# Kernel tuning notes

Measured on AMD Instinct MI355X. Metric: run time of the kernel, lower is better.

## Reference

```python
import jax, jax.numpy as jnp
import numpy as np

EPS = 1e-5
B, C, H, W = 64, 256, 64, 64


def _masked_mean(p9, r0, r1, c0, c1):
    # p9: [B,3,3,9,H,W]; r0,r1: [B,3] int row bounds (per i); c0,c1: [B,3] int col bounds (per j)
    Hh, Ww = p9.shape[-2], p9.shape[-1]
    rows = jnp.arange(Hh, dtype=jnp.int32)
    cols = jnp.arange(Ww, dtype=jnp.int32)
    mr = (rows[None, None, :] >= r0[..., None]) & (rows[None, None, :] < r1[..., None])  # [B,3,H]
    mc = (cols[None, None, :] >= c0[..., None]) & (cols[None, None, :] < c1[..., None])  # [B,3,W]
    mask = (mr[:, :, None, :, None] & mc[:, None, :, None, :]).astype(p9.dtype)  # [B,3,3,H,W]
    cnt = mask.sum((-2, -1))  # [B,3,3]
    s = jnp.einsum('bijkhw,bijhw->bijk', p9, mask)
    return jnp.where(cnt[..., None] > 0, s / jnp.maximum(cnt, 1.0)[..., None], 0.0)  # [B,3,3,9]


def _subj_obj_bounds(bbox, Hh, Ww):
    # bbox: [B,4] = [y0,y1,x0,x1] normalized
    y0, y1, x0, x1 = bbox[:, 0], bbox[:, 1], bbox[:, 2], bbox[:, 3]
    ch = (y1 - y0) / 3.0
    cw = (x1 - x0) / 3.0
    idx = jnp.arange(3, dtype=bbox.dtype)
    r0 = jnp.floor(Hh * (y0[:, None] + idx * ch[:, None])).astype(jnp.int32)
    r1 = jnp.floor(Hh * (y0[:, None] + (idx + 1.0) * ch[:, None])).astype(jnp.int32)
    dr = r1 <= r0
    r1n = jnp.where(dr & (r1 < Hh - 1), r1 + 1, r1)
    r0n = jnp.where(dr & (r1 >= Hh - 1), r0 - 1, r0)
    c0 = jnp.floor(Ww * (x0[:, None] + idx * cw[:, None])).astype(jnp.int32)
    c1 = jnp.floor(Ww * (x0[:, None] + (idx + 1.0) * cw[:, None])).astype(jnp.int32)
    dc = c1 <= c0
    c1n = jnp.where(dc & (c1 < Ww), c1 + 1, c1)
    c0n = jnp.where(dc & (c1 >= Ww), c0 - 1, c0)
    return r0n, r1n, c0n, c1n


def _joint_bounds(bbox, bbox_s, bbox_o, Hh, Ww):
    # intersection of bbox with the 3x3 cells of union(bbox_s, bbox_o)
    uy0 = jnp.minimum(bbox_s[:, 0], bbox_o[:, 0])
    uy1 = jnp.maximum(bbox_s[:, 1], bbox_o[:, 1])
    ux0 = jnp.minimum(bbox_s[:, 2], bbox_o[:, 2])
    ux1 = jnp.maximum(bbox_s[:, 3], bbox_o[:, 3])
    ch = (uy1 - uy0) / 3.0
    cw = (ux1 - ux0) / 3.0
    idx = jnp.arange(3, dtype=bbox.dtype)
    ylo = uy0[:, None] + idx * ch[:, None]
    yhi = uy0[:, None] + (idx + 1.0) * ch[:, None]
    xlo = ux0[:, None] + idx * cw[:, None]
    xhi = ux0[:, None] + (idx + 1.0) * cw[:, None]
    r0 = jnp.floor(Hh * jnp.maximum(bbox[:, 0][:, None], ylo)).astype(jnp.int32)
    r1 = jnp.floor(Hh * jnp.minimum(bbox[:, 1][:, None], yhi)).astype(jnp.int32)
    c0 = jnp.floor(Ww * jnp.maximum(bbox[:, 2][:, None], xlo)).astype(jnp.int32)
    c1 = jnp.floor(Ww * jnp.minimum(bbox[:, 3][:, None], xhi)).astype(jnp.int32)
    return r0, r1, c0, c1


def setup_inputs() -> dict:
    key = jax.random.key(0)
    ks = jax.random.split(key, 16)
    feat = jax.random.normal(ks[0], (B, C, H, W), dtype=jnp.float32)

    def make_bbox(k):
        k1, k2, k3, k4 = jax.random.split(k, 4)
        y0 = jax.random.uniform(k1, (B,), minval=0.0, maxval=0.4)
        y1 = jnp.minimum(y0 + jax.random.uniform(k2, (B,), minval=0.3, maxval=0.55), 0.99)
        x0 = jax.random.uniform(k3, (B,), minval=0.0, maxval=0.4)
        x1 = jnp.minimum(x0 + jax.random.uniform(k4, (B,), minval=0.3, maxval=0.55), 0.99)
        return jnp.stack([y0, y1, x0, x1], axis=1).astype(jnp.float32)

    bbox_s = make_bbox(ks[1])
    bbox_o = make_bbox(ks[2])
    predicate = jax.random.uniform(ks[3], (B, 9), dtype=jnp.float32)
    conv_w = jax.random.normal(ks[4], (324, 256), dtype=jnp.float32) * 0.02
    conv_b = jax.random.normal(ks[5], (324,), dtype=jnp.float32) * 0.02
    bn2_g = jax.random.uniform(ks[6], (324,), minval=0.5, maxval=1.5)
    bn2_b = jax.random.normal(ks[7], (324,)) * 0.02
    bn2_m = jax.random.normal(ks[8], (324,)) * 0.02
    bn2_v = jax.random.uniform(ks[9], (324,), minval=0.5, maxval=1.5)
    fc1_w = jax.random.normal(ks[10], (40, 81), dtype=jnp.float32) * 0.1
    fc1_b = jnp.zeros((40,), jnp.float32)
    bn1_g = jax.random.uniform(ks[11], (40,), minval=0.5, maxval=1.5)
    bn1_b = jax.random.normal(ks[12], (40,)) * 0.02
    bn1_m = jax.random.normal(ks[13], (40,)) * 0.02
    bn1_v = jax.random.uniform(ks[14], (40,), minval=0.5, maxval=1.5)
    fc2_w = jax.random.normal(ks[15], (9, 40), dtype=jnp.float32) * 0.1
    fc2_b = jnp.zeros((9,), jnp.float32)
    return dict(feat=feat, bbox_s=bbox_s, bbox_o=bbox_o, predicate=predicate,
                conv_w=conv_w, conv_b=conv_b, bn2_g=bn2_g, bn2_b=bn2_b, bn2_m=bn2_m, bn2_v=bn2_v,
                fc1_w=fc1_w, fc1_b=fc1_b, bn1_g=bn1_g, bn1_b=bn1_b, bn1_m=bn1_m, bn1_v=bn1_v,
                fc2_w=fc2_w, fc2_b=fc2_b)


def reference(feat, bbox_s, bbox_o, predicate, conv_w, conv_b, bn2_g, bn2_b, bn2_m, bn2_v,
              fc1_w, fc1_b, bn1_g, bn1_b, bn1_m, bn1_v, fc2_w, fc2_b):
    # 1x1 conv 256 -> 324, then BatchNorm2d (inference mode)
    prs = jnp.einsum('bchw,oc->bohw', feat, conv_w) + conv_b[None, :, None, None]
    prs = (prs - bn2_m[None, :, None, None]) * (bn2_g / jnp.sqrt(bn2_v + EPS))[None, :, None, None] + bn2_b[None, :, None, None]
    Bb, _, Hh, Ww = prs.shape
    # channel layout: start = i*27 + j*9 + k  ->  reshape to [B,3,3,9,H,W]
    def bank(lo):
        return prs[:, lo:lo + 81].reshape(Bb, 3, 3, 9, Hh, Ww)
    prs_s, prs_o, prs_js, prs_jo = bank(0), bank(81), bank(162), bank(243)

    feature_s = _masked_mean(prs_s, *_subj_obj_bounds(bbox_s, Hh, Ww))
    feature_o = _masked_mean(prs_o, *_subj_obj_bounds(bbox_o, Hh, Ww))
    feature_j = (_masked_mean(prs_js, *_joint_bounds(bbox_s, bbox_s, bbox_o, Hh, Ww)) +
                 _masked_mean(prs_jo, *_joint_bounds(bbox_o, bbox_s, bbox_o, Hh, Ww)))

    f = feature_s + feature_o + feature_j            # [B,3,3,9]
    f = jnp.transpose(f, (0, 3, 1, 2)).reshape(Bb, 81)  # torch layout [B,9,3,3] flattened

    h = f @ fc1_w.T + fc1_b
    h = (h - bn1_m) * (bn1_g / jnp.sqrt(bn1_v + EPS)) + bn1_b
    logits = h @ fc2_w.T + fc2_b
    return jnp.sum(logits * predicate, axis=1)
```

## Files before the change

kernel.cpp:

```cpp
#include <hip/hip_runtime.h>
#include <hip/hip_bf16.h>
#include <cstdint>

#define BB 64
#define CC 256
#define EPSF 1e-5f
#define PLANES 8
#define ZROW 24
#define SSTR 65
#define NPLANES (BB * CC)

__device__ __forceinline__ void region_bounds(int bank, int i, int j,
                                              float sy0, float sy1, float sx0, float sx1,
                                              float oy0, float oy1, float ox0, float ox1,
                                              int& r0, int& r1, int& c0, int& c1) {
    float fi = (float)i, fj = (float)j;
    if (bank < 2) {
        float y0 = bank ? oy0 : sy0, y1 = bank ? oy1 : sy1;
        float x0 = bank ? ox0 : sx0, x1 = bank ? ox1 : sx1;
        float ch = __fdiv_rn(__fsub_rn(y1, y0), 3.0f);
        float cw = __fdiv_rn(__fsub_rn(x1, x0), 3.0f);
        int R0 = (int)floorf(__fmul_rn(64.0f, __fadd_rn(y0, __fmul_rn(fi, ch))));
        int R1 = (int)floorf(__fmul_rn(64.0f, __fadd_rn(y0, __fmul_rn(__fadd_rn(fi, 1.0f), ch))));
        bool dr = (R1 <= R0);
        r1 = (dr && (R1 < 63)) ? R1 + 1 : R1;
        r0 = (dr && (R1 >= 63)) ? R0 - 1 : R0;
        int C0 = (int)floorf(__fmul_rn(64.0f, __fadd_rn(x0, __fmul_rn(fj, cw))));
        int C1 = (int)floorf(__fmul_rn(64.0f, __fadd_rn(x0, __fmul_rn(__fadd_rn(fj, 1.0f), cw))));
        bool dc = (C1 <= C0);
        c1 = (dc && (C1 < 64)) ? C1 + 1 : C1;
        c0 = (dc && (C1 >= 64)) ? C0 - 1 : C0;
    } else {
        float by0 = (bank == 2) ? sy0 : oy0, by1 = (bank == 2) ? sy1 : oy1;
        float bx0 = (bank == 2) ? sx0 : ox0, bx1 = (bank == 2) ? sx1 : ox1;
        float uy0 = fminf(sy0, oy0), uy1 = fmaxf(sy1, oy1);
        float ux0 = fminf(sx0, ox0), ux1 = fmaxf(sx1, ox1);
        float ch = __fdiv_rn(__fsub_rn(uy1, uy0), 3.0f);
        float cw = __fdiv_rn(__fsub_rn(ux1, ux0), 3.0f);
        float ylo = __fadd_rn(uy0, __fmul_rn(fi, ch));
        float yhi = __fadd_rn(uy0, __fmul_rn(__fadd_rn(fi, 1.0f), ch));
        float xlo = __fadd_rn(ux0, __fmul_rn(fj, cw));
        float xhi = __fadd_rn(ux0, __fmul_rn(__fadd_rn(fj, 1.0f), cw));
        r0 = (int)floorf(__fmul_rn(64.0f, fmaxf(by0, ylo)));
        r1 = (int)floorf(__fmul_rn(64.0f, fminf(by1, yhi)));
        c0 = (int)floorf(__fmul_rn(64.0f, fmaxf(bx0, xlo)));
        c1 = (int)floorf(__fmul_rn(64.0f, fminf(bx1, xhi)));
    }
}

__global__ __launch_bounds__(64, 4) void k_region_sums(const float* __restrict__ feat,
                                                       const float* __restrict__ bbox_s,
                                                       const float* __restrict__ bbox_o,
                                                       float* __restrict__ M) {
    int l = threadIdx.x;
    int pid0 = blockIdx.x * PLANES;
    int b = pid0 >> 8;

    float sy0 = bbox_s[b * 4 + 0], sy1 = bbox_s[b * 4 + 1];
    float sx0 = bbox_s[b * 4 + 2], sx1 = bbox_s[b * 4 + 3];
    float oy0 = bbox_o[b * 4 + 0], oy1 = bbox_o[b * 4 + 1];
    float ox0 = bbox_o[b * 4 + 2], ox1 = bbox_o[b * 4 + 3];

    int myb = l / 9, rest = l % 9, myi = rest / 3, myj = rest % 3;

    unsigned long long needm = 0ull, snapm = 0ull;
    int my_r0c = 0, my_r1c = 0, mycl = 0, mych = 0;
    bool colact = false;
    int cmin = 64;
    #pragma unroll
    for (int bk = 0; bk < 4; ++bk) {
        #pragma unroll
        for (int idx = 0; idx < 3; ++idx) {
            int r0, r1, c0, c1;
            region_bounds(bk, idx, idx, sy0, sy1, sx0, sx1, oy0, oy1, ox0, ox1,
                          r0, r1, c0, c1);
            int r0c = max(r0, 0), r1c = min(r1, 64);
            if (r1c > r0c) {
                unsigned long long hi = (r1c >= 64) ? ~0ull : ((1ull << r1c) - 1ull);
                unsigned long long lo = (1ull << r0c) - 1ull;
                needm |= hi ^ lo;
                snapm |= 1ull << (r1c - 1);
                if (r0c >= 1) snapm |= 1ull << (r0c - 1);
            }
            int clc = max(c0, 0), chc = min(c1, 64);
            if (chc > clc) {
                colact = colact || (l >= clc && l < chc);
                cmin = min(cmin, clc);
            }
            if (bk == myb && idx == myi) { my_r0c = r0c; my_r1c = r1c; }
            if (bk == myb && idx == myj) { mycl = max(c0, 0); mych = min(c1, 64); }
        }
    }
    {
        unsigned int a = __builtin_amdgcn_readfirstlane((unsigned int)needm);
        unsigned int bm = __builtin_amdgcn_readfirstlane((unsigned int)(needm >> 32));
        needm = (((unsigned long long)bm) << 32) | a;
        unsigned int c = __builtin_amdgcn_readfirstlane((unsigned int)snapm);
        unsigned int d = __builtin_amdgcn_readfirstlane((unsigned int)(snapm >> 32));
        snapm = (((unsigned long long)d) << 32) | c;
    }
    if (cmin >= 64) cmin = 0;
    int col_tgt = colact ? l : cmin;

    int cl = 0, chx = 0, idx0 = ZROW, idx1 = ZROW;
    if (l < 36) {
        cl = mycl; chx = mych;
        if (my_r1c <= my_r0c) {
            chx = cl;
        } else {
            idx1 = (int)__popcll(snapm & ((1ull << (my_r1c - 1)) - 1ull));
            idx0 = (my_r0c > 0) ? (int)__popcll(snapm & ((1ull << (my_r0c - 1)) - 1ull))
                                : ZROW;
        }
    }

    __shared__ float S[(ZROW + 1) * SSTR];
    S[ZROW * SSTR + l] = 0.0f;
    asm volatile("s_waitcnt lgkmcnt(0)" ::: "memory");

    const float* pfbase = feat + (size_t)pid0 * 4096 + col_tgt;
    float xA[32], xB[32];
    float run = 0.0f;
    int slot = 0;

#define ISSUE_H(X, Q)                                                       \
    do {                                                                    \
        const float* pp = pfbase + (size_t)((Q) >> 1) * 4096;               \
        const int h0 = ((Q) & 1) * 32;                                      \
        _Pragma("unroll")                                                   \
        for (int h = 0; h < 32; ++h) {                                      \
            if ((needm >> (h0 + h)) & 1ull) X[h] = pp[(h0 + h) * 64];       \
        }                                                                   \
    } while (0)

#define CONSUME_H(X, Q)                                                     \
    do {                                                                    \
        const int h0 = ((Q) & 1) * 32;                                      \
        if (h0 == 0) { run = 0.0f; slot = 0; }                              \
        _Pragma("unroll")                                                   \
        for (int h = 0; h < 32; ++h) {                                      \
            if ((needm >> (h0 + h)) & 1ull) run += X[h];                    \
            if ((snapm >> (h0 + h)) & 1ull) { S[slot * SSTR + l] = run; ++slot; } \
        }                                                                   \
    } while (0)

#define EVALP(P)                                                            \
    do {                                                                    \
        asm volatile("s_waitcnt lgkmcnt(0)" ::: "memory");                  \
        if (l < 36) {                                                       \
            float s = 0.0f;                                                 \
            for (int w = cl; w < chx; ++w)                                  \
                s += S[idx1 * SSTR + w] - S[idx0 * SSTR + w];               \
            M[(size_t)l * NPLANES + pid0 + (P)] = s;                        \
        }                                                                   \
        asm volatile("" ::: "memory");                                      \
    } while (0)

    ISSUE_H(xA, 0); ISSUE_H(xB, 1);
    CONSUME_H(xA, 0);  ISSUE_H(xA, 2);
    CONSUME_H(xB, 1);  ISSUE_H(xB, 3);   EVALP(0);
    CONSUME_H(xA, 2);  ISSUE_H(xA, 4);
    CONSUME_H(xB, 3);  ISSUE_H(xB, 5);   EVALP(1);
    CONSUME_H(xA, 4);  ISSUE_H(xA, 6);
    CONSUME_H(xB, 5);  ISSUE_H(xB, 7);   EVALP(2);
    CONSUME_H(xA, 6);  ISSUE_H(xA, 8);
    CONSUME_H(xB, 7);  ISSUE_H(xB, 9);   EVALP(3);
    CONSUME_H(xA, 8);  ISSUE_H(xA, 10);
    CONSUME_H(xB, 9);  ISSUE_H(xB, 11);  EVALP(4);
    CONSUME_H(xA, 10); ISSUE_H(xA, 12);
    CONSUME_H(xB, 11); ISSUE_H(xB, 13);  EVALP(5);
    CONSUME_H(xA, 12); ISSUE_H(xA, 14);
    CONSUME_H(xB, 13); ISSUE_H(xB, 15);  EVALP(6);
    CONSUME_H(xA, 14);
    CONSUME_H(xB, 15);                   EVALP(7);

#undef ISSUE_H
#undef CONSUME_H
#undef EVALP
}

__global__ __launch_bounds__(128) void k_head_dot(const float* __restrict__ M,
                                                  const float* __restrict__ bbox_s,
                                                  const float* __restrict__ bbox_o,
                                                  const float* __restrict__ conv_w,
                                                  const float* __restrict__ conv_b,
                                                  const float* __restrict__ g2,
                                                  const float* __restrict__ b2,
                                                  const float* __restrict__ m2,
                                                  const float* __restrict__ v2,
                                                  float* __restrict__ val) {
    int blk = blockIdx.x;
    int b = blk >> 2, bank = blk & 3;
    int t = threadIdx.x;

    __shared__ float MlT9[9 * 264];
    for (int i = t; i < 9 * 256; i += 128) {
        int ij = i >> 8, c = i & 255;
        MlT9[ij * 264 + c] = M[(size_t)(bank * 9 + ij) * NPLANES + (b << 8) + c];
    }
    __syncthreads();

    if (t < 81) {
        int ij = t / 9, k = t - ij * 9;
        int ii = ij / 3, jj = ij % 3;
        int o = bank * 81 + ii * 27 + jj * 9 + k;

        float sy0 = bbox_s[b * 4 + 0], sy1 = bbox_s[b * 4 + 1];
        float sx0 = bbox_s[b * 4 + 2], sx1 = bbox_s[b * 4 + 3];
        float oy0 = bbox_o[b * 4 + 0], oy1 = bbox_o[b * 4 + 1];
        float ox0 = bbox_o[b * 4 + 2], ox1 = bbox_o[b * 4 + 3];
        int r0, r1, c0, c1;
        region_bounds(bank, ii, jj, sy0, sy1, sx0, sx1, oy0, oy1, ox0, ox1,
                      r0, r1, c0, c1);
        int nrows = max(0, min(r1, 64) - max(r0, 0));
        int ncols = max(0, min(c1, 64) - max(c0, 0));
        float cnt = (float)(nrows * ncols);

        float v = 0.0f;
        if (cnt > 0.0f) {
            const float4* wv = (const float4*)(conv_w + o * 256);
            const float4* mv = (const float4*)(&MlT9[ij * 264]);
            float4 a4 = make_float4(0.f, 0.f, 0.f, 0.f);
            #pragma unroll 8
            for (int c4 = 0; c4 < 64; ++c4) {
                float4 wq = wv[c4], mq = mv[c4];
                a4.x += wq.x * mq.x; a4.y += wq.y * mq.y;
                a4.z += wq.z * mq.z; a4.w += wq.w * mq.w;
            }
            float dot = (a4.x + a4.y) + (a4.z + a4.w);
            float mean = dot / cnt;
            float sc = g2[o] / sqrtf(v2[o] + EPSF);
            v = (mean + conv_b[o] - m2[o]) * sc + b2[o];
        }
        val[b * 324 + bank * 81 + t] = v;
    }
}

__global__ __launch_bounds__(128) void k_head_mlp(const float* __restrict__ val,
                                                  const float* __restrict__ fc1_w,
                                                  const float* __restrict__ fc1_b,
                                                  const float* __restrict__ g1,
                                                  const float* __restrict__ b1,
                                                  const float* __restrict__ m1,
                                                  const float* __restrict__ v1,
                                                  const float* __restrict__ fc2_w,
                                                  const float* __restrict__ fc2_b,
                                                  const float* __restrict__ pred,
                                                  float* __restrict__ out) {
    int b = blockIdx.x;
    int t = threadIdx.x;

    __shared__ float fv[81];
    __shared__ float hv[40];
    __shared__ float lg[9];

    if (t < 81) {
        int k = t / 9, ij = t - k * 9;
        const float* vb = val + b * 324;
        fv[t] = vb[0 * 81 + ij * 9 + k] + vb[1 * 81 + ij * 9 + k] +
                vb[2 * 81 + ij * 9 + k] + vb[3 * 81 + ij * 9 + k];
    }
    __syncthreads();

    if (t < 40) {
        float h = fc1_b[t];
        for (int u = 0; u < 81; ++u) h += fv[u] * fc1_w[t * 81 + u];
        h = (h - m1[t]) * (g1[t] / sqrtf(v1[t] + EPSF)) + b1[t];
        hv[t] = h;
    }
    __syncthreads();

    if (t < 9) {
        float lgt = fc2_b[t];
        for (int u = 0; u < 40; ++u) lgt += hv[u] * fc2_w[t * 40 + u];
        lg[t] = lgt * pred[b * 9 + t];
    }
    __syncthreads();

    if (t == 0) {
        float s = 0.0f;
        for (int i = 0; i < 9; ++i) s += lg[i];
        out[b] = s;
    }
}

extern "C" void kernel_launch(void* const* d_in, const int* in_sizes, int n_in,
                              void* d_out, int out_size, void* d_ws, size_t ws_size,
                              hipStream_t stream) {
    const float* feat   = (const float*)d_in[0];
    const float* bbox_s = (const float*)d_in[1];
    const float* bbox_o = (const float*)d_in[2];
    const float* pred   = (const float*)d_in[3];
    const float* conv_w = (const float*)d_in[4];
    const float* conv_b = (const float*)d_in[5];
    const float* g2     = (const float*)d_in[6];
    const float* b2     = (const float*)d_in[7];
    const float* m2     = (const float*)d_in[8];
    const float* v2     = (const float*)d_in[9];
    const float* fc1_w  = (const float*)d_in[10];
    const float* fc1_b  = (const float*)d_in[11];
    const float* g1     = (const float*)d_in[12];
    const float* b1     = (const float*)d_in[13];
    const float* m1     = (const float*)d_in[14];
    const float* v1     = (const float*)d_in[15];
    const float* fc2_w  = (const float*)d_in[16];
    const float* fc2_b  = (const float*)d_in[17];
    float* out = (float*)d_out;

    char* ws = (char*)d_ws;
    float* M   = (float*)ws;
    float* val = (float*)(ws + 2359296);

    k_region_sums<<<(BB * CC) / PLANES, 64, 0, stream>>>(feat, bbox_s, bbox_o, M);
    k_head_dot<<<BB * 4, 128, 0, stream>>>(M, bbox_s, bbox_o, conv_w, conv_b,
                                           g2, b2, m2, v2, val);
    k_head_mlp<<<BB, 128, 0, stream>>>(val, fc1_w, fc1_b, g1, b1, m1, v1,
                                       fc2_w, fc2_b, pred, out);
}
```

Measured before the change: 61.90 us.

## Load 16-row chunks only for active row quarters and columns, 4 planes per block

Restructures the region-sum loads into 16-row chunks that are skipped entirely when no needed or snapshot row falls in that quarter of the plane. Lanes whose column is not used in any region now skip their loads instead of redirecting to a dummy column. Each block now handles 4 planes instead of 8, doubling the block count and using smaller register buffers. In exchange, rows inside an active quarter are loaded unconditionally, so some unneeded rows are fetched, and per-block setup runs twice as often.

```diff
diff --git a/kernel.cpp b/kernel.cpp
--- a/kernel.cpp
+++ b/kernel.cpp
@@ -5,7 +5,7 @@
 #define BB 64
 #define CC 256
 #define EPSF 1e-5f
-#define PLANES 8
+#define PLANES 4
 #define ZROW 24
 #define SSTR 65
 #define NPLANES (BB * CC)
@@ -66,7 +66,6 @@
     unsigned long long needm = 0ull, snapm = 0ull;
     int my_r0c = 0, my_r1c = 0, mycl = 0, mych = 0;
     bool colact = false;
-    int cmin = 64;
     #pragma unroll
     for (int bk = 0; bk < 4; ++bk) {
         #pragma unroll
@@ -83,10 +82,7 @@
                 if (r0c >= 1) snapm |= 1ull << (r0c - 1);
             }
             int clc = max(c0, 0), chc = min(c1, 64);
-            if (chc > clc) {
-                colact = colact || (l >= clc && l < chc);
-                cmin = min(cmin, clc);
-            }
+            if (chc > clc) colact = colact || (l >= clc && l < chc);
             if (bk == myb && idx == myi) { my_r0c = r0c; my_r1c = r1c; }
             if (bk == myb && idx == myj) { mycl = max(c0, 0); mych = min(c1, 64); }
         }
@@ -99,8 +95,11 @@
         unsigned int d = __builtin_amdgcn_readfirstlane((unsigned int)(snapm >> 32));
         snapm = (((unsigned long long)d) << 32) | c;
     }
-    if (cmin >= 64) cmin = 0;
-    int col_tgt = colact ? l : cmin;
+    unsigned long long useful = needm | snapm;
+    bool act[4] = { ((useful >>  0) & 0xFFFFull) != 0ull,
+                    ((useful >> 16) & 0xFFFFull) != 0ull,
+                    ((useful >> 32) & 0xFFFFull) != 0ull,
+                    ((useful >> 48) & 0xFFFFull) != 0ull };
 
     int cl = 0, chx = 0, idx0 = ZROW, idx1 = ZROW;
     if (l < 36) {
@@ -116,31 +115,38 @@
 
     __shared__ float S[(ZROW + 1) * SSTR];
     S[ZROW * SSTR + l] = 0.0f;
-    asm volatile("s_waitcnt lgkmcnt(0)" ::: "memory");
-
-    const float* pfbase = feat + (size_t)pid0 * 4096 + col_tgt;
-    float xA[32], xB[32];
+
+    const float* pfbase = feat + (size_t)pid0 * 4096 + l;
+    float xA[16], xB[16];
     float run = 0.0f;
     int slot = 0;
 
-#define ISSUE_H(X, Q)                                                       \
+#define ISSUE(SL, X)                                                        \
     do {                                                                    \
-        const float* pp = pfbase + (size_t)((Q) >> 1) * 4096;               \
-        const int h0 = ((Q) & 1) * 32;                                      \
-        _Pragma("unroll")                                                   \
-        for (int h = 0; h < 32; ++h) {                                      \
-            if ((needm >> (h0 + h)) & 1ull) X[h] = pp[(h0 + h) * 64];       \
+        const int cq_ = (SL) & 3;                                           \
+        if (act[cq_]) {                                                     \
+            const float* pp = pfbase + (size_t)((SL) >> 2) * 4096 + cq_ * 1024; \
+            _Pragma("unroll")                                               \
+            for (int h = 0; h < 16; ++h) {                                  \
+                float v = 0.0f;                                             \
+                if (colact) v = pp[h * 64];                                 \
+                X[h] = v;                                                   \
+            }                                                               \
         }                                                                   \
     } while (0)
 
-#define CONSUME_H(X, Q)                                                     \
+#define CONSUME(SL, X)                                                      \
     do {                                                                    \
-        const int h0 = ((Q) & 1) * 32;                                      \
-        if (h0 == 0) { run = 0.0f; slot = 0; }                              \
-        _Pragma("unroll")                                                   \
-        for (int h = 0; h < 32; ++h) {                                      \
-            if ((needm >> (h0 + h)) & 1ull) run += X[h];                    \
-            if ((snapm >> (h0 + h)) & 1ull) { S[slot * SSTR + l] = run; ++slot; } \
+        const int cq_ = (SL) & 3;                                           \
+        if (cq_ == 0) { run = 0.0f; slot = 0; }                             \
+        if (act[cq_]) {                                                     \
+            _Pragma("unroll")                                               \
+            for (int h = 0; h < 16; ++h) {                                  \
+                run += X[h];                                                \
+                if ((snapm >> (cq_ * 16 + h)) & 1ull) {                     \
+                    S[slot * SSTR + l] = run; ++slot;                       \
+                }                                                           \
+            }                                                               \
         }                                                                   \
     } while (0)
 
@@ -156,26 +162,26 @@
         asm volatile("" ::: "memory");                                      \
     } while (0)
 
-    ISSUE_H(xA, 0); ISSUE_H(xB, 1);
-    CONSUME_H(xA, 0);  ISSUE_H(xA, 2);
-    CONSUME_H(xB, 1);  ISSUE_H(xB, 3);   EVALP(0);
-    CONSUME_H(xA, 2);  ISSUE_H(xA, 4);
-    CONSUME_H(xB, 3);  ISSUE_H(xB, 5);   EVALP(1);
-    CONSUME_H(xA, 4);  ISSUE_H(xA, 6);
-    CONSUME_H(xB, 5);  ISSUE_H(xB, 7);   EVALP(2);
-    CONSUME_H(xA, 6);  ISSUE_H(xA, 8);
-    CONSUME_H(xB, 7);  ISSUE_H(xB, 9);   EVALP(3);
-    CONSUME_H(xA, 8);  ISSUE_H(xA, 10);
-    CONSUME_H(xB, 9);  ISSUE_H(xB, 11);  EVALP(4);
-    CONSUME_H(xA, 10); ISSUE_H(xA, 12);
-    CONSUME_H(xB, 11); ISSUE_H(xB, 13);  EVALP(5);
-    CONSUME_H(xA, 12); ISSUE_H(xA, 14);
-    CONSUME_H(xB, 13); ISSUE_H(xB, 15);  EVALP(6);
-    CONSUME_H(xA, 14);
-    CONSUME_H(xB, 15);                   EVALP(7);
-
-#undef ISSUE_H
-#undef CONSUME_H
+    ISSUE(0, xA);  ISSUE(1, xB);
+    CONSUME(0, xA);  ISSUE(2, xA);
+    CONSUME(1, xB);  ISSUE(3, xB);
+    CONSUME(2, xA);  ISSUE(4, xA);
+    CONSUME(3, xB);  ISSUE(5, xB);   EVALP(0);
+    CONSUME(4, xA);  ISSUE(6, xA);
+    CONSUME(5, xB);  ISSUE(7, xB);
+    CONSUME(6, xA);  ISSUE(8, xA);
+    CONSUME(7, xB);  ISSUE(9, xB);   EVALP(1);
+    CONSUME(8, xA);  ISSUE(10, xA);
+    CONSUME(9, xB);  ISSUE(11, xB);
+    CONSUME(10, xA); ISSUE(12, xA);
+    CONSUME(11, xB); ISSUE(13, xB);  EVALP(2);
+    CONSUME(12, xA); ISSUE(14, xA);
+    CONSUME(13, xB); ISSUE(15, xB);
+    CONSUME(14, xA);
+    CONSUME(15, xB);                 EVALP(3);
+
+#undef ISSUE
+#undef CONSUME
 #undef EVALP
 }
 
```

Result: faster. 57.06 us (-7.8%).
